# Performance work log

Measured on AMD Instinct MI355X. Metric: run time of the kernel, lower is better.

Reference implementation:

```python
import jax, jax.numpy as jnp
import numpy as np

N_NODES = 100000
N_REL = 4
N_EDGES = 600000
D = 128


def setup_inputs() -> dict:
    key = jax.random.key(0)
    k1, k2, k3 = jax.random.split(key, 3)
    edges = jax.random.randint(k1, (N_REL, 2, N_EDGES), 0, N_NODES, dtype=jnp.int32)
    X = jax.random.normal(k2, (N_NODES, D), dtype=jnp.float32)
    # one weight matrix per relation (GraphConv weight=True, bias=False)
    W = jax.random.normal(k3, (N_REL, D, D), dtype=jnp.float32) * (1.0 / np.sqrt(D))
    return {"edges": edges, "X": X, "W": W}


def _graphconv_both(src, dst, X, W):
    # DGL GraphConv, norm='both', no bias/activation, allow_zero_in_degree.
    ones = jnp.ones((src.shape[0],), dtype=X.dtype)
    deg_out = jax.ops.segment_sum(ones, src, num_segments=N_NODES).clip(1.0)
    deg_in = jax.ops.segment_sum(ones, dst, num_segments=N_NODES).clip(1.0)
    h = X * jax.lax.rsqrt(deg_out)[:, None]          # [N, D] src-normalized
    agg = jax.ops.segment_sum(h[src], dst, num_segments=N_NODES)  # SpMM: [N, D]
    agg = agg * jax.lax.rsqrt(deg_in)[:, None]
    return agg @ W                                   # dense transform [N, D]


def reference(edges, X, W):
    # sum of per-relation GraphConv outputs (stack(...).sum(0))
    Z = jnp.zeros((N_NODES, W.shape[-1]), dtype=X.dtype)
    for r in range(N_REL):  # small fixed relation count
        Z = Z + _graphconv_both(edges[r, 0], edges[r, 1], X, W[r])
    return Z
```

## Files before the change

### kernel.cpp

```cpp
#include <hip/hip_runtime.h>
#include <hip/hip_bf16.h>

constexpr int N_NODES = 100000;
constexpr int N_REL   = 4;
constexpr int N_EDGES = 600000;
constexpr int MAXDEG  = 32;
constexpr int D       = 128;
constexpr int KTOT    = N_REL * D;
constexpr int M_PAD   = 100096;

constexpr int NB   = 128;
constexpr int BW   = 784;
constexpr int NKEY = N_REL * NB;
constexpr int CAP  = 5632;
constexpr int EPB  = 2048;
constexpr int TOT_E   = N_REL * N_EDGES;
constexpr int P1_BLKS = (TOT_E + EPB - 1) / EPB;
constexpr int XC_BLKS = (N_NODES * D / 4) / 256;
constexpr int WC_BLKS = (N_REL * D * D) / 256;

typedef __attribute__((ext_vector_type(8))) short bf16x8;
typedef __attribute__((ext_vector_type(4))) float f32x4;

static __device__ __forceinline__ unsigned short f2bf(float f) {
    union { float f; unsigned int u; } v; v.f = f;
    unsigned int r = (v.u + 0x7fffu + ((v.u >> 16) & 1u)) >> 16;
    return (unsigned short)r;
}

__global__ __launch_bounds__(256) void pass1(const int* __restrict__ edges,
                                             int* __restrict__ gcur,
                                             uint2* __restrict__ bktd,
                                             unsigned* __restrict__ bkts,
                                             const float* __restrict__ X,
                                             unsigned short* __restrict__ Xb,
                                             const float* __restrict__ W,
                                             unsigned short* __restrict__ Wt) {
    int b = blockIdx.x;
    if (b < P1_BLKS) {
        __shared__ int hd[NKEY], hs[NKEY], bd[NKEY], bs[NKEY];
        int tid = threadIdx.x;
        for (int k = tid; k < NKEY; k += 256) { hd[k] = 0; hs[k] = 0; }
        __syncthreads();

        int e0 = b * EPB;
        int src[8], dst[8], kd[8], ks[8];
#pragma unroll
        for (int k = 0; k < 8; k++) {
            int t = e0 + k * 256 + tid;
            kd[k] = -1; ks[k] = -1; src[k] = 0; dst[k] = 0;
            if (t < TOT_E) {
                int r = t / N_EDGES;
                int e = t - r * N_EDGES;
                src[k] = edges[(size_t)(r * 2)     * N_EDGES + e];
                dst[k] = edges[(size_t)(r * 2 + 1) * N_EDGES + e];
                kd[k] = r * NB + dst[k] / BW;
                ks[k] = r * NB + src[k] / BW;
                atomicAdd(&hd[kd[k]], 1);
                atomicAdd(&hs[ks[k]], 1);
            }
        }
        __syncthreads();
        for (int k = tid; k < NKEY; k += 256) {
            int c = hd[k];
            bd[k] = c ? atomicAdd(&gcur[k * 16], c) : 0;
            hd[k] = 0;
            c = hs[k];
            bs[k] = c ? atomicAdd(&gcur[(NKEY + k) * 16], c) : 0;
            hs[k] = 0;
        }
        __syncthreads();
#pragma unroll
        for (int k = 0; k < 8; k++) {
            if (kd[k] >= 0) {
                int p = bd[kd[k]] + atomicAdd(&hd[kd[k]], 1);
                if (p < CAP) bktd[(size_t)kd[k] * CAP + p] = make_uint2((unsigned)src[k], (unsigned)dst[k]);
                p = bs[ks[k]] + atomicAdd(&hs[ks[k]], 1);
                if (p < CAP) bkts[(size_t)ks[k] * CAP + p] = (unsigned)src[k];
            }
        }
    } else if (b < P1_BLKS + XC_BLKS) {
        int t = (b - P1_BLKS) * 256 + threadIdx.x;
        float4 v = ((const float4*)X)[t];
        union { unsigned short u[4]; uint2 d; } o;
        o.u[0] = f2bf(v.x); o.u[1] = f2bf(v.y); o.u[2] = f2bf(v.z); o.u[3] = f2bf(v.w);
        ((uint2*)Xb)[t] = o.d;
    } else {
        int t = (b - P1_BLKS - XC_BLKS) * 256 + threadIdx.x;
        int r = t >> 14;
        int k = (t >> 7) & 127;
        int n = t & 127;
        Wt[(size_t)n * KTOT + r * D + k] = f2bf(W[t]);
    }
}

__global__ __launch_bounds__(1024) void pass2(const int* __restrict__ gcur,
                                              const uint2* __restrict__ bktd,
                                              const unsigned* __restrict__ bkts,
                                              int* __restrict__ esrc,
                                              int* __restrict__ indeg,
                                              float* __restrict__ routf) {
    __shared__ int cur[BW];
    int b = blockIdx.x, tid = threadIdx.x;
    if (tid < BW) cur[tid] = 0;
    __syncthreads();
    if (b < NKEY) {
        int key = b;
        int r = key >> 7;
        int node0 = (key - r * NB) * BW;
        int cnt = min(gcur[key * 16], CAP);
        for (int i = tid; i < cnt; i += 1024) {
            uint2 ed = bktd[(size_t)key * CAP + i];
            int pos = atomicAdd(&cur[(int)ed.y - node0], 1);
            if (pos < MAXDEG)
                esrc[((size_t)r * N_NODES + ed.y) * MAXDEG + pos] = (int)ed.x;
        }
        __syncthreads();
        int nN = min(BW, N_NODES - node0);
        if (tid < nN) indeg[r * N_NODES + node0 + tid] = cur[tid];
    } else {
        int key = b - NKEY;
        int r = key >> 7;
        int node0 = (key - r * NB) * BW;
        int cnt = min(gcur[(NKEY + key) * 16], CAP);
        for (int i = tid; i < cnt; i += 1024) {
            unsigned s = bkts[(size_t)key * CAP + i];
            atomicAdd(&cur[(int)s - node0], 1);
        }
        __syncthreads();
        int nN = min(BW, N_NODES - node0);
        if (tid < nN) {
            int c = cur[tid];
            routf[r * N_NODES + node0 + tid] = rsqrtf((float)(c < 1 ? 1 : c));
        }
    }
}

__global__ __launch_bounds__(256) void gather_ell(const int* __restrict__ esrc,
                                                  const int* __restrict__ indeg,
                                                  const float* __restrict__ routf,
                                                  const uint2* __restrict__ Xv,
                                                  uint2* __restrict__ A2) {
    __shared__ uint2 meta[8][N_REL][MAXDEG];
    int tid = threadIdx.x;
    int h   = tid >> 5;
    int l31 = tid & 31;
    int d   = blockIdx.x * 8 + h;

    int   n[N_REL];
    float rin[N_REL];
    int nm = 0;
#pragma unroll
    for (int r = 0; r < N_REL; r++) {
        int ind = indeg[r * N_NODES + d];
        n[r]   = ind > MAXDEG ? MAXDEG : ind;
        rin[r] = rsqrtf((float)(ind < 1 ? 1 : ind));
        nm = max(nm, n[r]);
        int s = 0; float c = 0.f;
        if (l31 < n[r]) {
            s = esrc[((size_t)r * N_NODES + d) * MAXDEG + l31];
            c = routf[r * N_NODES + s];
        }
        union { float f; unsigned u; } cu; cu.f = c;
        meta[h][r][l31] = make_uint2((unsigned)s, cu.u);
    }
    int nmax = max(nm, __shfl_xor(nm, 32));
    __syncthreads();

    float4 acc[N_REL];
#pragma unroll
    for (int r = 0; r < N_REL; r++) acc[r] = make_float4(0.f, 0.f, 0.f, 0.f);

#pragma unroll 2
    for (int i = 0; i < nmax; i++) {
        uint2 m[N_REL];
#pragma unroll
        for (int r = 0; r < N_REL; r++) m[r] = meta[h][r][i];
        uint2 v[N_REL];
#pragma unroll
        for (int r = 0; r < N_REL; r++)
            v[r] = Xv[(size_t)m[r].x * (D / 4) + l31];
#pragma unroll
        for (int r = 0; r < N_REL; r++) {
            union { unsigned u; float f; } cc; cc.u = m[r].y;
            union { unsigned u; float f; } a, b, e, g;
            a.u = v[r].x << 16; b.u = v[r].x & 0xFFFF0000u;
            e.u = v[r].y << 16; g.u = v[r].y & 0xFFFF0000u;
            acc[r].x += cc.f * a.f;
            acc[r].y += cc.f * b.f;
            acc[r].z += cc.f * e.f;
            acc[r].w += cc.f * g.f;
        }
    }

#pragma unroll
    for (int r = 0; r < N_REL; r++) {
        unsigned p0 = (unsigned)f2bf(rin[r] * acc[r].x) | ((unsigned)f2bf(rin[r] * acc[r].y) << 16);
        unsigned p1 = (unsigned)f2bf(rin[r] * acc[r].z) | ((unsigned)f2bf(rin[r] * acc[r].w) << 16);
        A2[(size_t)d * (KTOT / 4) + r * (D / 4) + l31] = make_uint2(p0, p1);
    }
}

__global__ __launch_bounds__(256) void gemm_mfma(const unsigned short* __restrict__ A,
                                                 const unsigned short* __restrict__ Wt,
                                                 float* __restrict__ Z) {
    int w    = threadIdx.x >> 6;
    int lane = threadIdx.x & 63;
    int l15  = lane & 15;
    int quad = lane >> 4;
    int row0 = blockIdx.x * 128 + w * 32;

    f32x4 acc[2][8];
#pragma unroll
    for (int m = 0; m < 2; m++)
#pragma unroll
        for (int j = 0; j < 8; j++) acc[m][j] = (f32x4){0.f, 0.f, 0.f, 0.f};

    for (int k0 = 0; k0 < KTOT; k0 += 32) {
        bf16x8 a[2];
#pragma unroll
        for (int m = 0; m < 2; m++)
            a[m] = *(const bf16x8*)(A + (size_t)(row0 + m * 16 + l15) * KTOT + k0 + quad * 8);
#pragma unroll
        for (int j = 0; j < 8; j++) {
            bf16x8 b = *(const bf16x8*)(Wt + (size_t)(j * 16 + l15) * KTOT + k0 + quad * 8);
            acc[0][j] = __builtin_amdgcn_mfma_f32_16x16x32_bf16(a[0], b, acc[0][j], 0, 0, 0);
            acc[1][j] = __builtin_amdgcn_mfma_f32_16x16x32_bf16(a[1], b, acc[1][j], 0, 0, 0);
        }
    }

#pragma unroll
    for (int m = 0; m < 2; m++)
#pragma unroll
        for (int reg = 0; reg < 4; reg++) {
            int row = row0 + m * 16 + quad * 4 + reg;
            if (row < N_NODES) {
#pragma unroll
                for (int j = 0; j < 8; j++)
                    Z[(size_t)row * D + j * 16 + l15] = acc[m][j][reg];
            }
        }
}

extern "C" void kernel_launch(void* const* d_in, const int* in_sizes, int n_in,
                              void* d_out, int out_size, void* d_ws, size_t ws_size,
                              hipStream_t stream) {
    const int*   edges = (const int*)d_in[0];
    const float* X     = (const float*)d_in[1];
    const float* W     = (const float*)d_in[2];
    float*       Z     = (float*)d_out;

    auto align256 = [](size_t x) { return (x + 255) & ~(size_t)255; };
    char* ws = (char*)d_ws;
    size_t off = 0;
    int* gcur          = (int*)(ws + off);            off = align256(off + (size_t)2 * NKEY * 16 * sizeof(int));
    int* indeg         = (int*)(ws + off);            off = align256(off + (size_t)N_REL * N_NODES * sizeof(int));
    float* routf       = (float*)(ws + off);          off = align256(off + (size_t)N_REL * N_NODES * sizeof(float));
    int* esrc          = (int*)(ws + off);            off = align256(off + (size_t)N_REL * N_NODES * MAXDEG * sizeof(int));
    unsigned short* Xb = (unsigned short*)(ws + off); off = align256(off + (size_t)N_NODES * D * sizeof(short));
    unsigned short* Wt = (unsigned short*)(ws + off); off = align256(off + (size_t)KTOT * D * sizeof(short));
    unsigned short* A  = (unsigned short*)(ws + off); off = align256(off + (size_t)M_PAD * KTOT * sizeof(short));
    uint2*    bktd = (uint2*)A;
    unsigned* bkts = (unsigned*)((char*)A + (size_t)NKEY * CAP * sizeof(uint2));

    hipMemsetAsync(gcur, 0, (size_t)2 * NKEY * 16 * sizeof(int), stream);

    pass1<<<P1_BLKS + XC_BLKS + WC_BLKS, 256, 0, stream>>>(
        edges, gcur, bktd, bkts, X, Xb, W, Wt);

    pass2<<<2 * NKEY, 1024, 0, stream>>>(gcur, bktd, bkts, esrc, indeg, routf);

    gather_ell<<<N_NODES / 8, 256, 0, stream>>>(
        esrc, indeg, routf, (const uint2*)Xb, (uint2*)A);

    gemm_mfma<<<M_PAD / 128, 256, 0, stream>>>(A, Wt, Z);
}
```

Baseline: 375.3 us.

## Feature-slice the SpMM gather and pre-pack source norms into ELL entries

After: 653.3 us. 1.74x slower.

```diff
diff --git a/kernel.cpp b/kernel.cpp
--- a/kernel.cpp
+++ b/kernel.cpp
@@ -8,6 +8,7 @@
 constexpr int D       = 128;
 constexpr int KTOT    = N_REL * D;
 constexpr int M_PAD   = 100096;
+constexpr int NSLC    = 8;
 
 constexpr int NB   = 128;
 constexpr int BW   = 784;
@@ -90,115 +91,125 @@
         int r = t >> 14;
         int k = (t >> 7) & 127;
         int n = t & 127;
-        Wt[(size_t)n * KTOT + r * D + k] = f2bf(W[t]);
-    }
-}
-
-__global__ __launch_bounds__(1024) void pass2(const int* __restrict__ gcur,
-                                              const uint2* __restrict__ bktd,
-                                              const unsigned* __restrict__ bkts,
-                                              int* __restrict__ esrc,
-                                              int* __restrict__ indeg,
-                                              float* __restrict__ routf) {
+        int s   = k >> 4;
+        int c16 = k & 15;
+        int j   = s * 64 + (c16 >> 1) * 8 + r * 2 + (c16 & 1);
+        Wt[(size_t)n * KTOT + j] = f2bf(W[t]);
+    }
+}
+
+__global__ __launch_bounds__(1024) void pass2a(const int* __restrict__ gcur,
+                                               const unsigned* __restrict__ bkts,
+                                               float* __restrict__ routf) {
     __shared__ int cur[BW];
     int b = blockIdx.x, tid = threadIdx.x;
     if (tid < BW) cur[tid] = 0;
     __syncthreads();
-    if (b < NKEY) {
-        int key = b;
-        int r = key >> 7;
-        int node0 = (key - r * NB) * BW;
-        int cnt = min(gcur[key * 16], CAP);
-        for (int i = tid; i < cnt; i += 1024) {
-            uint2 ed = bktd[(size_t)key * CAP + i];
-            int pos = atomicAdd(&cur[(int)ed.y - node0], 1);
-            if (pos < MAXDEG)
-                esrc[((size_t)r * N_NODES + ed.y) * MAXDEG + pos] = (int)ed.x;
-        }
-        __syncthreads();
-        int nN = min(BW, N_NODES - node0);
-        if (tid < nN) indeg[r * N_NODES + node0 + tid] = cur[tid];
-    } else {
-        int key = b - NKEY;
-        int r = key >> 7;
-        int node0 = (key - r * NB) * BW;
-        int cnt = min(gcur[(NKEY + key) * 16], CAP);
-        for (int i = tid; i < cnt; i += 1024) {
-            unsigned s = bkts[(size_t)key * CAP + i];
-            atomicAdd(&cur[(int)s - node0], 1);
-        }
-        __syncthreads();
-        int nN = min(BW, N_NODES - node0);
-        if (tid < nN) {
-            int c = cur[tid];
-            routf[r * N_NODES + node0 + tid] = rsqrtf((float)(c < 1 ? 1 : c));
-        }
-    }
-}
-
-__global__ __launch_bounds__(256) void gather_ell(const int* __restrict__ esrc,
-                                                  const int* __restrict__ indeg,
-                                                  const float* __restrict__ routf,
-                                                  const uint2* __restrict__ Xv,
-                                                  uint2* __restrict__ A2) {
-    __shared__ uint2 meta[8][N_REL][MAXDEG];
+    int r = b >> 7;
+    int node0 = (b & 127) * BW;
+    int cnt = min(gcur[(NKEY + b) * 16], CAP);
+    for (int i = tid; i < cnt; i += 1024)
+        atomicAdd(&cur[(int)bkts[(size_t)b * CAP + i] - node0], 1);
+    __syncthreads();
+    int nN = min(BW, N_NODES - node0);
+    if (tid < nN) {
+        int c = cur[tid];
+        routf[r * N_NODES + node0 + tid] = rsqrtf((float)(c < 1 ? 1 : c));
+    }
+}
+
+__global__ __launch_bounds__(1024) void pass2b(const int* __restrict__ gcur,
+                                               const uint2* __restrict__ bktd,
+                                               const float* __restrict__ routf,
+                                               uint2* __restrict__ esrcc,
+                                               int* __restrict__ indeg) {
+    __shared__ int cur[BW];
+    int b = blockIdx.x, tid = threadIdx.x;
+    if (tid < BW) cur[tid] = 0;
+    __syncthreads();
+    int r = b >> 7;
+    int node0 = (b & 127) * BW;
+    int cnt = min(gcur[b * 16], CAP);
+    for (int i = tid; i < cnt; i += 1024) {
+        uint2 ed = bktd[(size_t)b * CAP + i];
+        int pos = atomicAdd(&cur[(int)ed.y - node0], 1);
+        if (pos < MAXDEG) {
+            union { float f; unsigned u; } c; c.f = routf[r * N_NODES + (int)ed.x];
+            esrcc[((size_t)r * N_NODES + (int)ed.y) * MAXDEG + pos] = make_uint2(ed.x, c.u);
+        }
+    }
+    __syncthreads();
+    int nN = min(BW, N_NODES - node0);
+    if (tid < nN) indeg[r * N_NODES + node0 + tid] = cur[tid];
+}
+
+__global__ __launch_bounds__(256) void gather_sliced(const uint2* __restrict__ esrcc,
+                                                     const int* __restrict__ indeg,
+                                                     const unsigned* __restrict__ Xv,
+                                                     uint4* __restrict__ A4) {
+    __shared__ uint2 meta[N_REL][MAXDEG][32];
+    __shared__ float rinl[N_REL][32];
+    __shared__ short nds[N_REL][32];
+    __shared__ int   nmx[4];
     int tid = threadIdx.x;
-    int h   = tid >> 5;
-    int l31 = tid & 31;
-    int d   = blockIdx.x * 8 + h;
-
-    int   n[N_REL];
-    float rin[N_REL];
-    int nm = 0;
-#pragma unroll
-    for (int r = 0; r < N_REL; r++) {
-        int ind = indeg[r * N_NODES + d];
-        n[r]   = ind > MAXDEG ? MAXDEG : ind;
-        rin[r] = rsqrtf((float)(ind < 1 ? 1 : ind));
-        nm = max(nm, n[r]);
-        int s = 0; float c = 0.f;
-        if (l31 < n[r]) {
-            s = esrc[((size_t)r * N_NODES + d) * MAXDEG + l31];
-            c = routf[r * N_NODES + s];
-        }
-        union { float f; unsigned u; } cu; cu.f = c;
-        meta[h][r][l31] = make_uint2((unsigned)s, cu.u);
-    }
-    int nmax = max(nm, __shfl_xor(nm, 32));
-    __syncthreads();
-
-    float4 acc[N_REL];
-#pragma unroll
-    for (int r = 0; r < N_REL; r++) acc[r] = make_float4(0.f, 0.f, 0.f, 0.f);
-
-#pragma unroll 2
+    int s     = blockIdx.x & 7;
+    int node0 = (blockIdx.x >> 3) * 32;
+
+    if (tid < 4) nmx[tid] = 0;
+    __syncthreads();
+    if (tid < 128) {
+        int node = tid & 31, r = tid >> 5;
+        int ind = indeg[r * N_NODES + node0 + node];
+        int n = ind > MAXDEG ? MAXDEG : ind;
+        nds[r][node]  = (short)n;
+        rinl[r][node] = rsqrtf((float)(ind < 1 ? 1 : ind));
+        atomicMax(&nmx[node >> 3], n);
+    }
+    __syncthreads();
+    for (int idx = tid; idx < 4096; idx += 256) {
+        int slot = idx & 31, r = (idx >> 5) & 3, node = idx >> 7;
+        uint2 m = make_uint2(0u, 0u);
+        if (slot < (int)nds[r][node])
+            m = esrcc[((size_t)r * N_NODES + node0 + node) * MAXDEG + slot];
+        meta[r][slot][node] = m;
+    }
+    __syncthreads();
+
+    int node = tid >> 3;
+    int l7   = tid & 7;
+    int nmax = nmx[node >> 3];
+    const unsigned* Xp = Xv + (size_t)s * 8 + l7;
+
+    float2 acc[N_REL];
+#pragma unroll
+    for (int r = 0; r < N_REL; r++) acc[r] = make_float2(0.f, 0.f);
+
+#pragma unroll 4
     for (int i = 0; i < nmax; i++) {
         uint2 m[N_REL];
 #pragma unroll
-        for (int r = 0; r < N_REL; r++) m[r] = meta[h][r][i];
-        uint2 v[N_REL];
-#pragma unroll
-        for (int r = 0; r < N_REL; r++)
-            v[r] = Xv[(size_t)m[r].x * (D / 4) + l31];
+        for (int r = 0; r < N_REL; r++) m[r] = meta[r][i][node];
+        unsigned v[N_REL];
+#pragma unroll
+        for (int r = 0; r < N_REL; r++) v[r] = Xp[(size_t)m[r].x * (D / 2)];
 #pragma unroll
         for (int r = 0; r < N_REL; r++) {
             union { unsigned u; float f; } cc; cc.u = m[r].y;
-            union { unsigned u; float f; } a, b, e, g;
-            a.u = v[r].x << 16; b.u = v[r].x & 0xFFFF0000u;
-            e.u = v[r].y << 16; g.u = v[r].y & 0xFFFF0000u;
-            acc[r].x += cc.f * a.f;
-            acc[r].y += cc.f * b.f;
-            acc[r].z += cc.f * e.f;
-            acc[r].w += cc.f * g.f;
-        }
-    }
-
+            union { unsigned u; float f; } lo, hi;
+            lo.u = v[r] << 16;
+            hi.u = v[r] & 0xFFFF0000u;
+            acc[r].x += cc.f * lo.f;
+            acc[r].y += cc.f * hi.f;
+        }
+    }
+
+    unsigned o[N_REL];
 #pragma unroll
     for (int r = 0; r < N_REL; r++) {
-        unsigned p0 = (unsigned)f2bf(rin[r] * acc[r].x) | ((unsigned)f2bf(rin[r] * acc[r].y) << 16);
-        unsigned p1 = (unsigned)f2bf(rin[r] * acc[r].z) | ((unsigned)f2bf(rin[r] * acc[r].w) << 16);
-        A2[(size_t)d * (KTOT / 4) + r * (D / 4) + l31] = make_uint2(p0, p1);
-    }
+        float ri = rinl[r][node];
+        o[r] = (unsigned)f2bf(ri * acc[r].x) | ((unsigned)f2bf(ri * acc[r].y) << 16);
+    }
+    A4[(size_t)(node0 + node) * (KTOT / 8) + s * 8 + l7] = make_uint4(o[0], o[1], o[2], o[3]);
 }
 
 __global__ __launch_bounds__(256) void gemm_mfma(const unsigned short* __restrict__ A,
@@ -256,7 +267,7 @@
     int* gcur          = (int*)(ws + off);            off = align256(off + (size_t)2 * NKEY * 16 * sizeof(int));
     int* indeg         = (int*)(ws + off);            off = align256(off + (size_t)N_REL * N_NODES * sizeof(int));
     float* routf       = (float*)(ws + off);          off = align256(off + (size_t)N_REL * N_NODES * sizeof(float));
-    int* esrc          = (int*)(ws + off);            off = align256(off + (size_t)N_REL * N_NODES * MAXDEG * sizeof(int));
+    uint2* esrcc       = (uint2*)(ws + off);          off = align256(off + (size_t)N_REL * N_NODES * MAXDEG * sizeof(uint2));
     unsigned short* Xb = (unsigned short*)(ws + off); off = align256(off + (size_t)N_NODES * D * sizeof(short));
     unsigned short* Wt = (unsigned short*)(ws + off); off = align256(off + (size_t)KTOT * D * sizeof(short));
     unsigned short* A  = (unsigned short*)(ws + off); off = align256(off + (size_t)M_PAD * KTOT * sizeof(short));
@@ -268,10 +279,12 @@
     pass1<<<P1_BLKS + XC_BLKS + WC_BLKS, 256, 0, stream>>>(
         edges, gcur, bktd, bkts, X, Xb, W, Wt);
 
-    pass2<<<2 * NKEY, 1024, 0, stream>>>(gcur, bktd, bkts, esrc, indeg, routf);
-
-    gather_ell<<<N_NODES / 8, 256, 0, stream>>>(
-        esrc, indeg, routf, (const uint2*)Xb, (uint2*)A);
+    pass2a<<<NKEY, 1024, 0, stream>>>(gcur, bkts, routf);
+
+    pass2b<<<NKEY, 1024, 0, stream>>>(gcur, bktd, routf, esrcc, indeg);
+
+    gather_sliced<<<NSLC * (N_NODES / 32), 256, 0, stream>>>(
+        esrcc, indeg, (const unsigned*)Xb, (uint4*)A);
 
     gemm_mfma<<<M_PAD / 128, 256, 0, stream>>>(A, Wt, Z);
 }
```

## Pack dst bucket records and precompute src norm into ELL entries

Applied to the files above, without the earlier changes.

Result: faster. 363.6 us (-3.1%).

```diff
diff --git a/kernel.cpp b/kernel.cpp
--- a/kernel.cpp
+++ b/kernel.cpp
@@ -30,7 +30,7 @@
 
 __global__ __launch_bounds__(256) void pass1(const int* __restrict__ edges,
                                              int* __restrict__ gcur,
-                                             uint2* __restrict__ bktd,
+                                             unsigned* __restrict__ bktd,
                                              unsigned* __restrict__ bkts,
                                              const float* __restrict__ X,
                                              unsigned short* __restrict__ Xb,
@@ -73,8 +73,9 @@
 #pragma unroll
         for (int k = 0; k < 8; k++) {
             if (kd[k] >= 0) {
+                int dstloc = dst[k] - (kd[k] - (kd[k] >> 7) * NB) * BW;
                 int p = bd[kd[k]] + atomicAdd(&hd[kd[k]], 1);
-                if (p < CAP) bktd[(size_t)kd[k] * CAP + p] = make_uint2((unsigned)src[k], (unsigned)dst[k]);
+                if (p < CAP) bktd[(size_t)kd[k] * CAP + p] = (unsigned)src[k] | ((unsigned)dstloc << 17);
                 p = bs[ks[k]] + atomicAdd(&hs[ks[k]], 1);
                 if (p < CAP) bkts[(size_t)ks[k] * CAP + p] = (unsigned)src[k];
             }
@@ -94,51 +95,55 @@
     }
 }
 
-__global__ __launch_bounds__(1024) void pass2(const int* __restrict__ gcur,
-                                              const uint2* __restrict__ bktd,
-                                              const unsigned* __restrict__ bkts,
-                                              int* __restrict__ esrc,
-                                              int* __restrict__ indeg,
-                                              float* __restrict__ routf) {
+__global__ __launch_bounds__(1024) void pass2a(const int* __restrict__ gcur,
+                                               const unsigned* __restrict__ bkts,
+                                               float* __restrict__ routf) {
     __shared__ int cur[BW];
     int b = blockIdx.x, tid = threadIdx.x;
     if (tid < BW) cur[tid] = 0;
     __syncthreads();
-    if (b < NKEY) {
-        int key = b;
-        int r = key >> 7;
-        int node0 = (key - r * NB) * BW;
-        int cnt = min(gcur[key * 16], CAP);
-        for (int i = tid; i < cnt; i += 1024) {
-            uint2 ed = bktd[(size_t)key * CAP + i];
-            int pos = atomicAdd(&cur[(int)ed.y - node0], 1);
-            if (pos < MAXDEG)
-                esrc[((size_t)r * N_NODES + ed.y) * MAXDEG + pos] = (int)ed.x;
-        }
-        __syncthreads();
-        int nN = min(BW, N_NODES - node0);
-        if (tid < nN) indeg[r * N_NODES + node0 + tid] = cur[tid];
-    } else {
-        int key = b - NKEY;
-        int r = key >> 7;
-        int node0 = (key - r * NB) * BW;
-        int cnt = min(gcur[(NKEY + key) * 16], CAP);
-        for (int i = tid; i < cnt; i += 1024) {
-            unsigned s = bkts[(size_t)key * CAP + i];
-            atomicAdd(&cur[(int)s - node0], 1);
-        }
-        __syncthreads();
-        int nN = min(BW, N_NODES - node0);
-        if (tid < nN) {
-            int c = cur[tid];
-            routf[r * N_NODES + node0 + tid] = rsqrtf((float)(c < 1 ? 1 : c));
-        }
-    }
-}
-
-__global__ __launch_bounds__(256) void gather_ell(const int* __restrict__ esrc,
+    int r = b >> 7;
+    int node0 = (b & 127) * BW;
+    int cnt = min(gcur[(NKEY + b) * 16], CAP);
+    for (int i = tid; i < cnt; i += 1024)
+        atomicAdd(&cur[(int)bkts[(size_t)b * CAP + i] - node0], 1);
+    __syncthreads();
+    int nN = min(BW, N_NODES - node0);
+    if (tid < nN) {
+        int c = cur[tid];
+        routf[r * N_NODES + node0 + tid] = rsqrtf((float)(c < 1 ? 1 : c));
+    }
+}
+
+__global__ __launch_bounds__(1024) void pass2b(const int* __restrict__ gcur,
+                                               const unsigned* __restrict__ bktd,
+                                               const float* __restrict__ routf,
+                                               uint2* __restrict__ esrcc,
+                                               int* __restrict__ indeg) {
+    __shared__ int cur[BW];
+    int b = blockIdx.x, tid = threadIdx.x;
+    if (tid < BW) cur[tid] = 0;
+    __syncthreads();
+    int r = b >> 7;
+    int node0 = (b & 127) * BW;
+    int cnt = min(gcur[b * 16], CAP);
+    for (int i = tid; i < cnt; i += 1024) {
+        unsigned rec = bktd[(size_t)b * CAP + i];
+        int s      = (int)(rec & 0x1FFFFu);
+        int dstloc = (int)(rec >> 17);
+        int pos = atomicAdd(&cur[dstloc], 1);
+        if (pos < MAXDEG) {
+            union { float f; unsigned u; } c; c.f = routf[r * N_NODES + s];
+            esrcc[((size_t)r * N_NODES + node0 + dstloc) * MAXDEG + pos] = make_uint2((unsigned)s, c.u);
+        }
+    }
+    __syncthreads();
+    int nN = min(BW, N_NODES - node0);
+    if (tid < nN) indeg[r * N_NODES + node0 + tid] = cur[tid];
+}
+
+__global__ __launch_bounds__(256) void gather_ell(const uint2* __restrict__ esrcc,
                                                   const int* __restrict__ indeg,
-                                                  const float* __restrict__ routf,
                                                   const uint2* __restrict__ Xv,
                                                   uint2* __restrict__ A2) {
     __shared__ uint2 meta[8][N_REL][MAXDEG];
@@ -156,13 +161,10 @@
         n[r]   = ind > MAXDEG ? MAXDEG : ind;
         rin[r] = rsqrtf((float)(ind < 1 ? 1 : ind));
         nm = max(nm, n[r]);
-        int s = 0; float c = 0.f;
-        if (l31 < n[r]) {
-            s = esrc[((size_t)r * N_NODES + d) * MAXDEG + l31];
-            c = routf[r * N_NODES + s];
-        }
-        union { float f; unsigned u; } cu; cu.f = c;
-        meta[h][r][l31] = make_uint2((unsigned)s, cu.u);
+        uint2 m = make_uint2(0u, 0u);
+        if (l31 < n[r])
+            m = esrcc[((size_t)r * N_NODES + d) * MAXDEG + l31];
+        meta[h][r][l31] = m;
     }
     int nmax = max(nm, __shfl_xor(nm, 32));
     __syncthreads();
@@ -171,7 +173,7 @@
 #pragma unroll
     for (int r = 0; r < N_REL; r++) acc[r] = make_float4(0.f, 0.f, 0.f, 0.f);
 
-#pragma unroll 2
+#pragma unroll 4
     for (int i = 0; i < nmax; i++) {
         uint2 m[N_REL];
 #pragma unroll
@@ -256,22 +258,24 @@
     int* gcur          = (int*)(ws + off);            off = align256(off + (size_t)2 * NKEY * 16 * sizeof(int));
     int* indeg         = (int*)(ws + off);            off = align256(off + (size_t)N_REL * N_NODES * sizeof(int));
     float* routf       = (float*)(ws + off);          off = align256(off + (size_t)N_REL * N_NODES * sizeof(float));
-    int* esrc          = (int*)(ws + off);            off = align256(off + (size_t)N_REL * N_NODES * MAXDEG * sizeof(int));
+    uint2* esrcc       = (uint2*)(ws + off);          off = align256(off + (size_t)N_REL * N_NODES * MAXDEG * sizeof(uint2));
     unsigned short* Xb = (unsigned short*)(ws + off); off = align256(off + (size_t)N_NODES * D * sizeof(short));
     unsigned short* Wt = (unsigned short*)(ws + off); off = align256(off + (size_t)KTOT * D * sizeof(short));
     unsigned short* A  = (unsigned short*)(ws + off); off = align256(off + (size_t)M_PAD * KTOT * sizeof(short));
-    uint2*    bktd = (uint2*)A;
-    unsigned* bkts = (unsigned*)((char*)A + (size_t)NKEY * CAP * sizeof(uint2));
+    unsigned* bktd = (unsigned*)A;
+    unsigned* bkts = (unsigned*)((char*)A + (size_t)NKEY * CAP * sizeof(unsigned));
 
     hipMemsetAsync(gcur, 0, (size_t)2 * NKEY * 16 * sizeof(int), stream);
 
     pass1<<<P1_BLKS + XC_BLKS + WC_BLKS, 256, 0, stream>>>(
         edges, gcur, bktd, bkts, X, Xb, W, Wt);
 
-    pass2<<<2 * NKEY, 1024, 0, stream>>>(gcur, bktd, bkts, esrc, indeg, routf);
+    pass2a<<<NKEY, 1024, 0, stream>>>(gcur, bkts, routf);
+
+    pass2b<<<NKEY, 1024, 0, stream>>>(gcur, bktd, routf, esrcc, indeg);
 
     gather_ell<<<N_NODES / 8, 256, 0, stream>>>(
-        esrc, indeg, routf, (const uint2*)Xb, (uint2*)A);
+        esrcc, indeg, (const uint2*)Xb, (uint2*)A);
 
     gemm_mfma<<<M_PAD / 128, 256, 0, stream>>>(A, Wt, Z);
 }
```
